# Kernel tuning notes

Hardware: AMD Instinct MI355X
Metric: run time of the kernel (lower is better)

## Reference

```python
import jax, jax.numpy as jnp
import numpy as np

B, S, E, H = 4, 2048, 1024, 16
DH = E // H


def setup_inputs() -> dict:
    key = jax.random.key(0)
    ks = jax.random.split(key, 8)
    sc = 0.02
    inp = {
        "v": jax.random.normal(ks[0], (B, S, E), jnp.float32),
        "k": jax.random.normal(ks[1], (B, S, E), jnp.float32),
        "q": jax.random.normal(ks[2], (B, S, E), jnp.float32),
        # causal mask, broadcast over batch and heads; 0 => masked
        "mask": jnp.tril(jnp.ones((S, S), jnp.int32))[None, None, :, :],
        "wq": jax.random.normal(ks[3], (E, E), jnp.float32) * sc,
        "bq": jnp.zeros((E,), jnp.float32),
        "wk": jax.random.normal(ks[4], (E, E), jnp.float32) * sc,
        "bk": jnp.zeros((E,), jnp.float32),
        "wv": jax.random.normal(ks[5], (E, E), jnp.float32) * sc,
        "bv": jnp.zeros((E,), jnp.float32),
        "wo": jax.random.normal(ks[6], (E, E), jnp.float32) * sc,
        "bo": jnp.zeros((E,), jnp.float32),
    }
    return inp


def _split_heads(x):
    # [B,S,E] -> [B,H,S,DH]
    b, s, _ = x.shape
    return x.reshape(b, s, H, DH).transpose(0, 2, 1, 3)


def reference(v, k, q, mask, wq, bq, wk, bk, wv, bv, wo, bo):
    # Linear layers (torch Linear: x @ W^T + b)
    qh = _split_heads(q @ wq.T + bq)
    kh = _split_heads(k @ wk.T + bk)
    vh = _split_heads(v @ wv.T + bv)
    scale = 1.0 / jnp.sqrt(jnp.asarray(DH, qh.dtype))
    scores = jnp.einsum("bhqd,bhkd->bhqk", qh, kh) * scale  # [B,H,S,S]
    scores = jnp.where(mask == 0, -jnp.inf, scores)
    attn = jax.nn.softmax(scores, axis=-1)
    # dropout p=0.0 -> identity
    x = jnp.einsum("bhqk,bhkd->bhqd", attn, vh)  # [B,H,S,DH]
    x = x.transpose(0, 2, 1, 3).reshape(x.shape[0], -1, E)  # [B,S,E]
    return x @ wo.T + bo
```

## Files before the change

### kernel.cpp

```cpp
#include <hip/hip_runtime.h>
#include <hip/hip_bf16.h>

#define B_  4
#define S_  2048
#define E_  1024
#define H_  16
#define DH_ 64
constexpr int M_ = B_ * S_;
constexpr int K_ = E_;
constexpr int N_ = E_;
constexpr long NE_ = (long)B_ * S_ * E_;
constexpr long EE_ = (long)E_ * E_;

typedef __attribute__((ext_vector_type(8))) short bf16x8;
typedef __attribute__((ext_vector_type(4))) float f32x4;

__device__ __forceinline__ unsigned short f2bf(float f) {
    union { float f; unsigned u; } a; a.f = f;
    unsigned u = a.u;
    return (unsigned short)((u + 0x7fffu + ((u >> 16) & 1u)) >> 16);
}
__device__ __forceinline__ unsigned short f2bf_fast(float f) {
    union { float f; unsigned u; } a; a.f = f;
    return (unsigned short)((a.u + 0x8000u) >> 16);
}

__device__ __forceinline__ void async_copy16(const unsigned short* g, unsigned short* l) {
    __builtin_amdgcn_global_load_lds(
        (const __attribute__((address_space(1))) void*)g,
        (__attribute__((address_space(3))) void*)l, 16, 0, 0);
}

__global__ void cast3(const float* __restrict__ i0, const float* __restrict__ i1,
                      const float* __restrict__ i2,
                      unsigned short* __restrict__ o0, unsigned short* __restrict__ o1,
                      unsigned short* __restrict__ o2, int n4) {
    const float* in = blockIdx.y == 0 ? i0 : (blockIdx.y == 1 ? i1 : i2);
    unsigned short* out = blockIdx.y == 0 ? o0 : (blockIdx.y == 1 ? o1 : o2);
    int i = blockIdx.x * blockDim.x + threadIdx.x;
    if (i >= n4) return;
    float4 v = ((const float4*)in)[i];
    ushort4 o;
    o.x = f2bf(v.x); o.y = f2bf(v.y); o.z = f2bf(v.z); o.w = f2bf(v.w);
    ((ushort4*)out)[i] = o;
}

__global__ void cast4(const float* __restrict__ i0, const float* __restrict__ i1,
                      const float* __restrict__ i2, const float* __restrict__ i3,
                      unsigned short* __restrict__ o0, unsigned short* __restrict__ o1,
                      unsigned short* __restrict__ o2, unsigned short* __restrict__ o3,
                      int n4) {
    int y = blockIdx.y;
    const float* in = y == 0 ? i0 : (y == 1 ? i1 : (y == 2 ? i2 : i3));
    unsigned short* out = y == 0 ? o0 : (y == 1 ? o1 : (y == 2 ? o2 : o3));
    int i = blockIdx.x * blockDim.x + threadIdx.x;
    if (i >= n4) return;
    float4 v = ((const float4*)in)[i];
    ushort4 o;
    o.x = f2bf(v.x); o.y = f2bf(v.y); o.z = f2bf(v.z); o.w = f2bf(v.w);
    ((ushort4*)out)[i] = o;
}

__device__ __forceinline__ void gemm_core(
    const unsigned short* __restrict__ A, const unsigned short* __restrict__ Bw,
    unsigned short* sA, unsigned short* sB, int bm, int bn,
    int wave, int lane, f32x4 (*acc)[4]) {
    const int lane15 = lane & 15;
    const int laneq  = lane >> 4;
    const int waveM = wave & 1, waveN = wave >> 1;
    const int lrow = lane >> 3;
    const int lcol = (lane & 7) * 8;

    for (int k0 = 0; k0 < K_; k0 += 64) {
        __syncthreads();
        for (int c = wave; c < 16; c += 4) {
            const unsigned short* gA = A + (long)(bm * 128 + c * 8 + lrow) * K_ + k0 + lcol;
            async_copy16(gA, &sA[c * 512]);
            const unsigned short* gB = Bw + (long)(bn * 128 + c * 8 + lrow) * K_ + k0 + lcol;
            async_copy16(gB, &sB[c * 512]);
        }
        __syncthreads();
#pragma unroll
        for (int ks = 0; ks < 2; ++ks) {
            const int kc = ks * 32 + laneq * 8;
            bf16x8 af[4], bfr[4];
#pragma unroll
            for (int mi = 0; mi < 4; ++mi)
                af[mi] = *(const bf16x8*)&sA[(waveM * 64 + mi * 16 + lane15) * 64 + kc];
#pragma unroll
            for (int ni = 0; ni < 4; ++ni)
                bfr[ni] = *(const bf16x8*)&sB[(waveN * 64 + ni * 16 + lane15) * 64 + kc];
#pragma unroll
            for (int mi = 0; mi < 4; ++mi)
#pragma unroll
                for (int ni = 0; ni < 4; ++ni)
                    acc[mi][ni] = __builtin_amdgcn_mfma_f32_16x16x32_bf16(
                        af[mi], bfr[ni], acc[mi][ni], 0, 0, 0);
        }
    }
}

__global__ __launch_bounds__(256, 2)
void gemm3(const unsigned short* __restrict__ A0, const unsigned short* __restrict__ A1,
           const unsigned short* __restrict__ A2,
           const unsigned short* __restrict__ W0, const unsigned short* __restrict__ W1,
           const unsigned short* __restrict__ W2,
           const float* __restrict__ b0, const float* __restrict__ b1,
           const float* __restrict__ b2,
           unsigned short* __restrict__ o0, unsigned short* __restrict__ o1,
           unsigned short* __restrict__ o2, float osc0) {
    __shared__ __align__(16) unsigned short sA[128 * 64];
    __shared__ __align__(16) unsigned short sB[128 * 64];
    const int z = blockIdx.z;
    const unsigned short* A  = z == 0 ? A0 : (z == 1 ? A1 : A2);
    const unsigned short* Bw = z == 0 ? W0 : (z == 1 ? W1 : W2);
    const float* bias        = z == 0 ? b0 : (z == 1 ? b1 : b2);
    unsigned short* Out      = z == 0 ? o0 : (z == 1 ? o1 : o2);
    const float oscale = z == 0 ? osc0 : 1.0f;

    const int tid = threadIdx.x, wave = tid >> 6, lane = tid & 63;
    const int lane15 = lane & 15, laneq = lane >> 4;
    const int bm = blockIdx.x, bn = blockIdx.y;
    const int waveM = wave & 1, waveN = wave >> 1;

    f32x4 acc[4][4] = {};
    gemm_core(A, Bw, sA, sB, bm, bn, wave, lane, acc);

#pragma unroll
    for (int mi = 0; mi < 4; ++mi) {
        const int mbase = bm * 128 + waveM * 64 + mi * 16 + laneq * 4;
#pragma unroll
        for (int ni = 0; ni < 4; ++ni) {
            const int n = bn * 128 + waveN * 64 + ni * 16 + lane15;
            const float bv = bias[n];
            if (z == 2) {
                const int b = mbase >> 11, s = mbase & (S_ - 1);
                const int h = n >> 6, d = n & (DH_ - 1);
                const long idx = ((long)(b * H_ + h) * DH_ + d) * S_ + s;
                ushort4 o;
                o.x = f2bf(acc[mi][ni][0] + bv);
                o.y = f2bf(acc[mi][ni][1] + bv);
                o.z = f2bf(acc[mi][ni][2] + bv);
                o.w = f2bf(acc[mi][ni][3] + bv);
                *(ushort4*)&Out[idx] = o;
            } else {
#pragma unroll
                for (int r = 0; r < 4; ++r) {
                    const int m = mbase + r;
                    const float v = (acc[mi][ni][r] + bv) * oscale;
                    const int b = m >> 11, s = m & (S_ - 1);
                    const int h = n >> 6, d = n & (DH_ - 1);
                    const long idx = ((long)(b * H_ + h) * S_ + s) * DH_ + d;
                    Out[idx] = f2bf(v);
                }
            }
        }
    }
}

__global__ __launch_bounds__(256, 2)
void gemm_out(const unsigned short* __restrict__ A, const unsigned short* __restrict__ Bw,
              const float* __restrict__ bias, float* __restrict__ Out) {
    __shared__ __align__(16) unsigned short sA[128 * 64];
    __shared__ __align__(16) unsigned short sB[128 * 64];
    const int tid = threadIdx.x, wave = tid >> 6, lane = tid & 63;
    const int lane15 = lane & 15, laneq = lane >> 4;
    const int bm = blockIdx.x, bn = blockIdx.y;
    const int waveM = wave & 1, waveN = wave >> 1;

    f32x4 acc[4][4] = {};
    gemm_core(A, Bw, sA, sB, bm, bn, wave, lane, acc);

#pragma unroll
    for (int mi = 0; mi < 4; ++mi) {
        const int mbase = bm * 128 + waveM * 64 + mi * 16 + laneq * 4;
#pragma unroll
        for (int ni = 0; ni < 4; ++ni) {
            const int n = bn * 128 + waveN * 64 + ni * 16 + lane15;
            const float bv = bias[n];
#pragma unroll
            for (int r = 0; r < 4; ++r)
                Out[(long)(mbase + r) * N_ + n] = acc[mi][ni][r] + bv;
        }
    }
}

constexpr int ALDK = 72;

__device__ __forceinline__ int swz(int row, int col) {
    return row * 64 + (col ^ (((row >> 1) & 7) << 3));
}

template <bool DIAG>
__device__ __forceinline__ void attn_tile(
    const bf16x8* qf, const unsigned short* sK, const unsigned short* sV,
    unsigned short* sP, int wave, int lane15, int laneq,
    f32x4* o_acc, float* rs) {
    f32x4 sc[4] = {};
#pragma unroll
    for (int ks = 0; ks < 2; ++ks) {
#pragma unroll
        for (int ct = 0; ct < 4; ++ct) {
            bf16x8 kf = *(const bf16x8*)&sK[swz(ct * 16 + lane15, ks * 32 + laneq * 8)];
            sc[ct] = __builtin_amdgcn_mfma_f32_16x16x32_bf16(qf[ks], kf, sc[ct], 0, 0, 0);
        }
    }
    const int prow = wave * 16 + laneq * 4;
#pragma unroll
    for (int ct = 0; ct < 4; ++ct) {
        const int colg = ct * 16 + lane15;
#pragma unroll
        for (int r = 0; r < 4; ++r) {
            float s = sc[ct][r];
            if (DIAG) {
                if (colg > prow + r) s = -1e30f;
            }
            const float p = __builtin_amdgcn_exp2f(s);
            rs[r] += p;
            sP[swz(prow + r, colg)] = f2bf_fast(p);
        }
    }
#pragma unroll
    for (int ks = 0; ks < 2; ++ks) {
        bf16x8 pf = *(const bf16x8*)&sP[swz(wave * 16 + lane15, ks * 32 + laneq * 8)];
#pragma unroll
        for (int dt = 0; dt < 4; ++dt) {
            bf16x8 vf = *(const bf16x8*)&sV[swz(dt * 16 + lane15, ks * 32 + laneq * 8)];
            o_acc[dt] = __builtin_amdgcn_mfma_f32_16x16x32_bf16(pf, vf, o_acc[dt], 0, 0, 0);
        }
    }
}

__global__ __launch_bounds__(256, 4)
void attn_kernel(const unsigned short* __restrict__ qh,
                 const unsigned short* __restrict__ kh,
                 const unsigned short* __restrict__ vT,
                 unsigned short* __restrict__ ctx) {
    __shared__ __align__(16) unsigned short sK[2][64 * ALDK];
    __shared__ __align__(16) unsigned short sV[2][64 * ALDK];
    __shared__ __align__(16) unsigned short sP[64 * ALDK];

    const int tid = threadIdx.x;
    const int wave = tid >> 6, lane = tid & 63;
    const int lane15 = lane & 15, laneq = lane >> 4;
    const int x = blockIdx.x;
    const int qta = x, qtb = 31 - x;
    const int bh = blockIdx.y;
    const long headQ = (long)bh * S_ * DH_;
    const long headV = (long)bh * DH_ * S_;
    const int q0a = qta * 64, q0b = qtb * 64;

    bf16x8 qfA[2], qfB[2];
    {
        const unsigned short* qa = qh + headQ + (long)(q0a + wave * 16 + lane15) * DH_;
        qfA[0] = *(const bf16x8*)(qa + laneq * 8);
        qfA[1] = *(const bf16x8*)(qa + 32 + laneq * 8);
        const unsigned short* qbp = qh + headQ + (long)(q0b + wave * 16 + lane15) * DH_;
        qfB[0] = *(const bf16x8*)(qbp + laneq * 8);
        qfB[1] = *(const bf16x8*)(qbp + 32 + laneq * 8);
    }

    f32x4 oA[4] = {}, oB[4] = {};
    float rsA[4] = {0.f, 0.f, 0.f, 0.f}, rsB[4] = {0.f, 0.f, 0.f, 0.f};

    const int r0 = tid >> 3;
    const int c0 = (tid & 7) * 8;

    const int ktmax = qtb + 1;

    {
        const unsigned short* kbase = kh + headQ;
        *(bf16x8*)&sK[0][swz(r0, c0)]      = *(const bf16x8*)(kbase + (long)r0 * DH_ + c0);
        *(bf16x8*)&sK[0][swz(32 + r0, c0)] = *(const bf16x8*)(kbase + (long)(32 + r0) * DH_ + c0);
        const unsigned short* vbase = vT + headV;
        *(bf16x8*)&sV[0][swz(r0, c0)]      = *(const bf16x8*)(vbase + (long)r0 * S_ + c0);
        *(bf16x8*)&sV[0][swz(32 + r0, c0)] = *(const bf16x8*)(vbase + (long)(32 + r0) * S_ + c0);
    }

    for (int kt = 0; kt < ktmax; ++kt) {
        const int cur = kt & 1, nxt = cur ^ 1;
        __syncthreads();

        bf16x8 kr0, kr1, vr0, vr1;
        const bool pfn = (kt + 1 < ktmax);
        if (pfn) {
            const int k0n = (kt + 1) * 64;
            const unsigned short* kbase = kh + headQ + (long)k0n * DH_;
            kr0 = *(const bf16x8*)(kbase + (long)r0 * DH_ + c0);
            kr1 = *(const bf16x8*)(kbase + (long)(32 + r0) * DH_ + c0);
            const unsigned short* vbase = vT + headV + k0n;
            vr0 = *(const bf16x8*)(vbase + (long)r0 * S_ + c0);
            vr1 = *(const bf16x8*)(vbase + (long)(32 + r0) * S_ + c0);
        }

        if (kt == qtb)
            attn_tile<true >(qfB, sK[cur], sV[cur], sP, wave, lane15, laneq, oB, rsB);
        else
            attn_tile<false>(qfB, sK[cur], sV[cur], sP, wave, lane15, laneq, oB, rsB);

        if (kt <= qta) {
            if (kt == qta)
                attn_tile<true >(qfA, sK[cur], sV[cur], sP, wave, lane15, laneq, oA, rsA);
            else
                attn_tile<false>(qfA, sK[cur], sV[cur], sP, wave, lane15, laneq, oA, rsA);
        }

        if (pfn) {
            *(bf16x8*)&sK[nxt][swz(r0, c0)]      = kr0;
            *(bf16x8*)&sK[nxt][swz(32 + r0, c0)] = kr1;
            *(bf16x8*)&sV[nxt][swz(r0, c0)]      = vr0;
            *(bf16x8*)&sV[nxt][swz(32 + r0, c0)] = vr1;
        }
    }

    float lA[4], lB[4];
#pragma unroll
    for (int r = 0; r < 4; ++r) {
        float va = rsA[r];
        va += __shfl_xor(va, 1); va += __shfl_xor(va, 2);
        va += __shfl_xor(va, 4); va += __shfl_xor(va, 8);
        lA[r] = va;
        float vb = rsB[r];
        vb += __shfl_xor(vb, 1); vb += __shfl_xor(vb, 2);
        vb += __shfl_xor(vb, 4); vb += __shfl_xor(vb, 8);
        lB[r] = vb;
    }

    const int b = bh >> 4, h = bh & 15;
#pragma unroll
    for (int dt = 0; dt < 4; ++dt) {
        const int d = h * 64 + dt * 16 + lane15;
#pragma unroll
        for (int r = 0; r < 4; ++r) {
            const int rowo = wave * 16 + laneq * 4 + r;
            ctx[((long)b * S_ + q0a + rowo) * E_ + d] = f2bf(oA[dt][r] / lA[r]);
            ctx[((long)b * S_ + q0b + rowo) * E_ + d] = f2bf(oB[dt][r] / lB[r]);
        }
    }
}

extern "C" void kernel_launch(void* const* d_in, const int* in_sizes, int n_in,
                              void* d_out, int out_size, void* d_ws, size_t ws_size,
                              hipStream_t stream) {
    const float* v_in = (const float*)d_in[0];
    const float* k_in = (const float*)d_in[1];
    const float* q_in = (const float*)d_in[2];
    const float* wq = (const float*)d_in[4];
    const float* bq = (const float*)d_in[5];
    const float* wk = (const float*)d_in[6];
    const float* bk = (const float*)d_in[7];
    const float* wv = (const float*)d_in[8];
    const float* bv = (const float*)d_in[9];
    const float* wo = (const float*)d_in[10];
    const float* bo = (const float*)d_in[11];

    unsigned short* qb   = (unsigned short*)d_ws;
    unsigned short* kb   = qb + NE_;
    unsigned short* vb   = kb + NE_;
    unsigned short* wqb  = vb + NE_;
    unsigned short* wkb  = wqb + EE_;
    unsigned short* wvb  = wkb + EE_;
    unsigned short* wob  = wvb + EE_;
    unsigned short* qhb  = wob + EE_;
    unsigned short* khb  = qhb + NE_;
    unsigned short* vTb  = khb + NE_;
    unsigned short* ctxb = qb;

    const int n4a = (int)(NE_ / 4);
    const int n4w = (int)(EE_ / 4);
    cast3<<<dim3(n4a / 256, 3), 256, 0, stream>>>(q_in, k_in, v_in, qb, kb, vb, n4a);
    cast4<<<dim3(n4w / 256, 4), 256, 0, stream>>>(wq, wk, wv, wo, wqb, wkb, wvb, wob, n4w);

    const float QSCALE = 0.125f * 1.44269504089f;

    gemm3<<<dim3(M_ / 128, N_ / 128, 3), 256, 0, stream>>>(
        qb, kb, vb, wqb, wkb, wvb, bq, bk, bv, qhb, khb, vTb, QSCALE);

    attn_kernel<<<dim3(16, B_ * H_), 256, 0, stream>>>(qhb, khb, vTb, ctxb);

    gemm_out<<<dim3(M_ / 128, N_ / 128), 256, 0, stream>>>(ctxb, wob, bo, (float*)d_out);
}
```

Baseline: 349.6 us.

## Double-buffer GEMM LDS tiles with BK=32 to overlap loads and MFMA

Restructures the shared GEMM core used by the QKV projection and output projection kernels into a two-stage ping-pong pipeline. The K step shrinks from 64 to 32 so two buffers fit in the same LDS footprint. The next tile's async global-to-LDS copy is issued before computing on the current tile, which leaves one barrier per iteration instead of two. This is meant to hide global load latency behind MFMA work, at the cost of twice as many loop iterations and barriers, a new LDS row stride, and less MFMA work per barrier.

```diff
diff --git a/kernel.cpp b/kernel.cpp
--- a/kernel.cpp
+++ b/kernel.cpp
@@ -61,42 +61,57 @@
     ((ushort4*)out)[i] = o;
 }
 
+constexpr int BK  = 32;
+constexpr int TSZ = 128 * BK;
+
+__device__ __forceinline__ void stage_ops(
+    const unsigned short* __restrict__ A, const unsigned short* __restrict__ Bw,
+    long bmrow, long bnrow, int k0,
+    unsigned short* sA, unsigned short* sB, int wave, int lane) {
+    const int row = lane >> 2;
+    const int col = (lane & 3) * 8;
+#pragma unroll
+    for (int c = 0; c < 2; ++c) {
+        const int chunk = wave * 2 + c;
+        const long r = chunk * 16 + row;
+        async_copy16(A + (bmrow + r) * K_ + k0 + col, sA + chunk * 512);
+        async_copy16(Bw + (bnrow + r) * K_ + k0 + col, sB + chunk * 512);
+    }
+}
+
 __device__ __forceinline__ void gemm_core(
     const unsigned short* __restrict__ A, const unsigned short* __restrict__ Bw,
-    unsigned short* sA, unsigned short* sB, int bm, int bn,
-    int wave, int lane, f32x4 (*acc)[4]) {
+    unsigned short* sA, unsigned short* sB,
+    int bm, int bn, int wave, int lane, f32x4 (*acc)[4]) {
     const int lane15 = lane & 15;
     const int laneq  = lane >> 4;
     const int waveM = wave & 1, waveN = wave >> 1;
-    const int lrow = lane >> 3;
-    const int lcol = (lane & 7) * 8;
-
-    for (int k0 = 0; k0 < K_; k0 += 64) {
+    const long bmrow = (long)bm * 128, bnrow = (long)bn * 128;
+
+    stage_ops(A, Bw, bmrow, bnrow, 0, sA, sB, wave, lane);
+
+    int cur = 0;
+    for (int k0 = 0; k0 < K_; k0 += BK) {
         __syncthreads();
-        for (int c = wave; c < 16; c += 4) {
-            const unsigned short* gA = A + (long)(bm * 128 + c * 8 + lrow) * K_ + k0 + lcol;
-            async_copy16(gA, &sA[c * 512]);
-            const unsigned short* gB = Bw + (long)(bn * 128 + c * 8 + lrow) * K_ + k0 + lcol;
-            async_copy16(gB, &sB[c * 512]);
-        }
-        __syncthreads();
-#pragma unroll
-        for (int ks = 0; ks < 2; ++ks) {
-            const int kc = ks * 32 + laneq * 8;
-            bf16x8 af[4], bfr[4];
-#pragma unroll
-            for (int mi = 0; mi < 4; ++mi)
-                af[mi] = *(const bf16x8*)&sA[(waveM * 64 + mi * 16 + lane15) * 64 + kc];
+        if (k0 + BK < K_)
+            stage_ops(A, Bw, bmrow, bnrow, k0 + BK,
+                      sA + (cur ^ 1) * TSZ, sB + (cur ^ 1) * TSZ, wave, lane);
+        const unsigned short* cA = sA + cur * TSZ;
+        const unsigned short* cB = sB + cur * TSZ;
+        bf16x8 af[4], bfr[4];
+#pragma unroll
+        for (int mi = 0; mi < 4; ++mi)
+            af[mi] = *(const bf16x8*)&cA[(waveM * 64 + mi * 16 + lane15) * BK + laneq * 8];
+#pragma unroll
+        for (int ni = 0; ni < 4; ++ni)
+            bfr[ni] = *(const bf16x8*)&cB[(waveN * 64 + ni * 16 + lane15) * BK + laneq * 8];
+#pragma unroll
+        for (int mi = 0; mi < 4; ++mi)
 #pragma unroll
             for (int ni = 0; ni < 4; ++ni)
-                bfr[ni] = *(const bf16x8*)&sB[(waveN * 64 + ni * 16 + lane15) * 64 + kc];
-#pragma unroll
-            for (int mi = 0; mi < 4; ++mi)
-#pragma unroll
-                for (int ni = 0; ni < 4; ++ni)
-                    acc[mi][ni] = __builtin_amdgcn_mfma_f32_16x16x32_bf16(
-                        af[mi], bfr[ni], acc[mi][ni], 0, 0, 0);
-        }
+                acc[mi][ni] = __builtin_amdgcn_mfma_f32_16x16x32_bf16(
+                    af[mi], bfr[ni], acc[mi][ni], 0, 0, 0);
+        cur ^= 1;
     }
 }
 
@@ -109,8 +124,8 @@
            const float* __restrict__ b2,
            unsigned short* __restrict__ o0, unsigned short* __restrict__ o1,
            unsigned short* __restrict__ o2, float osc0) {
-    __shared__ __align__(16) unsigned short sA[128 * 64];
-    __shared__ __align__(16) unsigned short sB[128 * 64];
+    __shared__ __align__(16) unsigned short sA[2 * TSZ];
+    __shared__ __align__(16) unsigned short sB[2 * TSZ];
     const int z = blockIdx.z;
     const unsigned short* A  = z == 0 ? A0 : (z == 1 ? A1 : A2);
     const unsigned short* Bw = z == 0 ? W0 : (z == 1 ? W1 : W2);
@@ -161,8 +176,8 @@
 __global__ __launch_bounds__(256, 2)
 void gemm_out(const unsigned short* __restrict__ A, const unsigned short* __restrict__ Bw,
               const float* __restrict__ bias, float* __restrict__ Out) {
-    __shared__ __align__(16) unsigned short sA[128 * 64];
-    __shared__ __align__(16) unsigned short sB[128 * 64];
+    __shared__ __align__(16) unsigned short sA[2 * TSZ];
+    __shared__ __align__(16) unsigned short sB[2 * TSZ];
     const int tid = threadIdx.x, wave = tid >> 6, lane = tid & 63;
     const int lane15 = lane & 15, laneq = lane >> 4;
     const int bm = blockIdx.x, bn = blockIdx.y;
```

Result: no change. 355.7 us (+1.7%).
